# Optimization experiments

Measured on AMD Instinct MI355X. Metric: run time of the kernel, lower is better.

## Reference

```python
import jax, jax.numpy as jnp
import numpy as np

# ---- static problem configuration (mirrors Barrier_Net param) ----
B, NN, NO, SD = 100000, 16, 8, 4        # agents, neighbors, obstacles, state dim
H, PHI_OUT, ADIM = 64, 16, 2            # MLP hidden, deepset latent, action dim
DS, B_GAMMA, B_EXPH = 0.2, 0.01, 1.0    # r_safe, barrier gain, barrier exponent
PHI_MIN, PHI_MAX = -1.0, 1.0            # empty-action range
A_MIN, A_MAX = -2.0, 2.0                # final action range
D_OBS = 1 + (NN + 1) * SD + 2 * NO      # 85


def mlp2(x, w1, b1, w2, b2):
    return jax.nn.relu(x @ w1 + b1) @ w2 + b2


def setup_inputs() -> dict:
    key = jax.random.key(0)
    ks = jax.random.split(key, 10)
    x = jax.random.normal(ks[0], (B, D_OBS), jnp.float32)
    x = x.at[:, 0].set(float(NN))  # first entry encodes the neighbor count

    def w(k, shape):
        return jax.random.normal(k, shape, jnp.float32) * 0.1

    return {
        "x": x,
        "phi_w1": w(ks[1], (SD, H)), "phi_b1": jnp.zeros((H,), jnp.float32),
        "phi_w2": w(ks[2], (H, PHI_OUT)), "phi_b2": jnp.zeros((PHI_OUT,), jnp.float32),
        "obs_w1": w(ks[3], (2, H)), "obs_b1": jnp.zeros((H,), jnp.float32),
        "obs_w2": w(ks[4], (H, PHI_OUT)), "obs_b2": jnp.zeros((PHI_OUT,), jnp.float32),
        "rho_w1": w(ks[5], (PHI_OUT, H)), "rho_b1": jnp.zeros((H,), jnp.float32),
        "rho_w2": w(ks[6], (H, ADIM)), "rho_b2": jnp.zeros((ADIM,), jnp.float32),
        "psi_w1": w(ks[7], (ADIM + 2, H)), "psi_b1": jnp.zeros((H,), jnp.float32),
        "psi_w2": w(ks[8], (H, ADIM)), "psi_b2": jnp.zeros((ADIM,), jnp.float32),
    }


def reference(x, phi_w1, phi_b1, phi_w2, phi_b2, obs_w1, obs_b1, obs_w2, obs_b2,
              rho_w1, rho_b1, rho_w2, rho_b2, psi_w1, psi_b1, psi_w2, psi_b2):
    # observation layout: [nn, self(SD), nn relative neighbor states(SD each), no obstacles(2 each)]
    nb = x[:, 1 + SD:1 + SD + NN * SD].reshape(B, NN, SD)   # relative neighbor states
    ob = x[:, 1 + (NN + 1) * SD:].reshape(B, NO, 2)          # relative obstacle positions

    # --- DeepSet: permutation-invariant sum of phi over elements, then rho ---
    phi_sum = mlp2(nb, phi_w1, phi_b1, phi_w2, phi_b2).sum(axis=1)   # [B, PHI_OUT]
    obs_sum = mlp2(ob, obs_w1, obs_b1, obs_w2, obs_b2).sum(axis=1)   # [B, PHI_OUT]
    rho = mlp2(phi_sum + obs_sum, rho_w1, rho_b1, rho_w2, rho_b2)    # [B, ADIM]

    # --- empty(): psi head on cat(rho, g) with tanh range squash to [phi_min, phi_max] ---
    g = x[:, 0:2]
    e = mlp2(jnp.concatenate([rho, g], axis=1), psi_w1, psi_b1, psi_w2, psi_b2)
    empty = (jnp.tanh(e) + 1.0) * 0.5 * (PHI_MAX - PHI_MIN) + PHI_MIN

    # --- barrier: gather neighbor rel-positions, scalar potential, scatter-add per agent ---
    p_ij = -nb[..., 0:2]                                    # [B, NN, 2], p^i - p^j
    h_ij = jnp.linalg.norm(p_ij, axis=-1) - DS              # [B, NN]
    barrier = jnp.sum((B_GAMMA / h_ij ** B_EXPH)[..., None] * p_ij, axis=1)  # [B, 2]

    action = jnp.tanh(empty + barrier)
    return (action + 1.0) * 0.5 * (A_MAX - A_MIN) + A_MIN
```

## Files before the change

kernel.cpp:

```cpp
#include <hip/hip_runtime.h>

#define BATCH 100000

typedef float v2 __attribute__((ext_vector_type(2)));

__device__ __forceinline__ v2 fma2(v2 a, v2 b, v2 c) { return __builtin_elementwise_fma(a, b, c); }
__device__ __forceinline__ v2 relu2(v2 a) { v2 z = {0.f, 0.f}; return __builtin_elementwise_max(a, z); }
__device__ __forceinline__ v2 splat(float a) { v2 r = {a, a}; return r; }
__device__ __forceinline__ v2 ldv2(const float* p) { return *(const v2*)p; }

__global__ __launch_bounds__(256, 4) void barrier_net(
    const float* __restrict__ x,
    const float* __restrict__ phi_w1, const float* __restrict__ phi_b1,
    const float* __restrict__ phi_w2, const float* __restrict__ phi_b2,
    const float* __restrict__ obs_w1, const float* __restrict__ obs_b1,
    const float* __restrict__ obs_w2, const float* __restrict__ obs_b2,
    const float* __restrict__ rho_w1, const float* __restrict__ rho_b1,
    const float* __restrict__ rho_w2, const float* __restrict__ rho_b2,
    const float* __restrict__ psi_w1, const float* __restrict__ psi_b1,
    const float* __restrict__ psi_w2, const float* __restrict__ psi_b2,
    float2* __restrict__ out)
{
    __shared__ float accL[2][2][32][16];
    __shared__ float rrL[2][2][32][2];
    __shared__ float eeL[2][2][32][2];

    const int lane = threadIdx.x & 63;
    const int wave = threadIdx.x >> 6;
    const int pair = wave >> 1;
    const int h    = wave & 1;
    const int kk   = lane >> 1;
    const int t    = lane & 1;
    int s = blockIdx.x * 64 + pair * 32 + kk;
    const bool valid = (s < BATCH);
    if (!valid) s = BATCH - 1;
    const float* xr = x + (size_t)s * 85;

    const int HB = __builtin_amdgcn_readfirstlane(h) * 32;
    const float* pw1 = phi_w1 + HB;
    const float* pb1 = phi_b1 + HB;
    const float* pw2 = phi_w2 + (size_t)HB * 16;
    const float* qw1 = obs_w1 + HB;
    const float* qb1 = obs_b1 + HB;
    const float* qw2 = obs_w2 + (size_t)HB * 16;
    const float* rw1 = rho_w1 + HB;
    const float* rb1 = rho_b1 + HB;
    const float* rw2 = rho_w2 + (size_t)HB * 2;
    const float* sw1 = psi_w1 + HB;
    const float* sb1 = psi_b1 + HB;
    const float* sw2 = psi_w2 + (size_t)HB * 2;

    float nb[8][4];
    const int nbase = 5 + 32 * t;
#pragma unroll
    for (int n = 0; n < 8; ++n)
#pragma unroll
        for (int k = 0; k < 4; ++k)
            nb[n][k] = xr[nbase + 4 * n + k];

    float bar0 = 0.f, bar1 = 0.f;
    if (h == 0) {
#pragma unroll
        for (int n = 0; n < 8; ++n) {
            float p0 = -nb[n][0], p1 = -nb[n][1];
            float r  = __builtin_amdgcn_sqrtf(fmaf(p0, p0, p1 * p1));
            float sc = 0.01f * __builtin_amdgcn_rcpf(r - 0.2f);
            bar0 = fmaf(sc, p0, bar0);
            bar1 = fmaf(sc, p1, bar1);
        }
        bar0 += __shfl_xor(bar0, 1);
        bar1 += __shfl_xor(bar1, 1);
    }

    v2 acc[8];
#pragma unroll
    for (int p = 0; p < 8; ++p)
        acc[p] = fma2(splat(4.f), ldv2(phi_b2 + 2 * p),
                 fma2(splat(2.f), ldv2(obs_b2 + 2 * p), splat(0.f)));

#pragma unroll 2
    for (int c = 0; c < 4; ++c) {
        const int hb = 8 * c;
        v2 hsv[4] = {{0.f,0.f},{0.f,0.f},{0.f,0.f},{0.f,0.f}};
#pragma unroll
        for (int n = 0; n < 8; ++n) {
#pragma unroll
            for (int p = 0; p < 4; ++p) {
                v2 tv = fma2(splat(nb[n][0]), ldv2(pw1 + hb + 2 * p),
                        fma2(splat(nb[n][1]), ldv2(pw1 + 64 + hb + 2 * p),
                        fma2(splat(nb[n][2]), ldv2(pw1 + 128 + hb + 2 * p),
                        fma2(splat(nb[n][3]), ldv2(pw1 + 192 + hb + 2 * p),
                                              ldv2(pb1 + hb + 2 * p)))));
                hsv[p] += relu2(tv);
            }
        }
#pragma unroll
        for (int p = 0; p < 4; ++p) {
            const float* r0 = pw2 + (size_t)(hb + 2 * p) * 16;
            v2 hx = splat(hsv[p].x), hy = splat(hsv[p].y);
#pragma unroll
            for (int q = 0; q < 8; ++q)
                acc[q] = fma2(hy, ldv2(r0 + 16 + 2 * q),
                         fma2(hx, ldv2(r0 + 2 * q), acc[q]));
        }
    }

    float ob[4][2];
    const int obase = 69 + 8 * t;
#pragma unroll
    for (int o = 0; o < 4; ++o) {
        ob[o][0] = xr[obase + 2 * o];
        ob[o][1] = xr[obase + 2 * o + 1];
    }

#pragma unroll 2
    for (int c = 0; c < 4; ++c) {
        const int hb = 8 * c;
        v2 hsv[4] = {{0.f,0.f},{0.f,0.f},{0.f,0.f},{0.f,0.f}};
#pragma unroll
        for (int o = 0; o < 4; ++o) {
#pragma unroll
            for (int p = 0; p < 4; ++p) {
                v2 tv = fma2(splat(ob[o][0]), ldv2(qw1 + hb + 2 * p),
                        fma2(splat(ob[o][1]), ldv2(qw1 + 64 + hb + 2 * p),
                                              ldv2(qb1 + hb + 2 * p)));
                hsv[p] += relu2(tv);
            }
        }
#pragma unroll
        for (int p = 0; p < 4; ++p) {
            const float* r0 = qw2 + (size_t)(hb + 2 * p) * 16;
            v2 hx = splat(hsv[p].x), hy = splat(hsv[p].y);
#pragma unroll
            for (int q = 0; q < 8; ++q)
                acc[q] = fma2(hy, ldv2(r0 + 16 + 2 * q),
                         fma2(hx, ldv2(r0 + 2 * q), acc[q]));
        }
    }

#pragma unroll
    for (int p = 0; p < 8; ++p) {
        acc[p].x += __shfl_xor(acc[p].x, 1);
        acc[p].y += __shfl_xor(acc[p].y, 1);
    }

    {
        float* slot = &accL[pair][h][kk][8 * t];
#pragma unroll
        for (int p = 0; p < 4; ++p) {
            v2 lo = acc[p], hi = acc[p + 4];
            v2 sel;
            sel.x = t ? hi.x : lo.x;
            sel.y = t ? hi.y : lo.y;
            *(v2*)(slot + 2 * p) = sel;
        }
    }
    __syncthreads();
    {
        const float* oslot = &accL[pair][h ^ 1][kk][0];
#pragma unroll
        for (int p = 0; p < 8; ++p)
            acc[p] += ldv2(oslot + 2 * p);
    }

    const float g0 = xr[0], g1 = xr[1];

    v2 rr = (h == 0) ? ldv2(rho_b2) : splat(0.f);
#pragma unroll 2
    for (int c = 0; c < 4; ++c) {
        const int hb = 8 * c;
        v2 tt[4];
#pragma unroll
        for (int p = 0; p < 4; ++p)
            tt[p] = ldv2(rb1 + hb + 2 * p);
#pragma unroll
        for (int j = 0; j < 8; ++j) {
            v2 ax = splat(acc[j].x), ay = splat(acc[j].y);
            const float* rj0 = rw1 + (size_t)(2 * j) * 64 + hb;
            const float* rj1 = rw1 + (size_t)(2 * j + 1) * 64 + hb;
#pragma unroll
            for (int p = 0; p < 4; ++p)
                tt[p] = fma2(ay, ldv2(rj1 + 2 * p),
                        fma2(ax, ldv2(rj0 + 2 * p), tt[p]));
        }
#pragma unroll
        for (int p = 0; p < 4; ++p) {
            v2 u = relu2(tt[p]);
            rr = fma2(splat(u.x), ldv2(rw2 + 2 * (hb + 2 * p)), rr);
            rr = fma2(splat(u.y), ldv2(rw2 + 2 * (hb + 2 * p) + 2), rr);
        }
    }
    rrL[pair][h][kk][t] = t ? rr.y : rr.x;
    __syncthreads();
    {
        v2 rro = ldv2(&rrL[pair][h ^ 1][kk][0]);
        rr += rro;
    }

    v2 ee = (h == 0) ? ldv2(psi_b2) : splat(0.f);
#pragma unroll 2
    for (int c = 0; c < 4; ++c) {
        const int hb = 8 * c;
#pragma unroll
        for (int p = 0; p < 4; ++p) {
            v2 tv = fma2(splat(rr.x), ldv2(sw1 + hb + 2 * p),
                    fma2(splat(rr.y), ldv2(sw1 + 64 + hb + 2 * p),
                    fma2(splat(g0),   ldv2(sw1 + 128 + hb + 2 * p),
                    fma2(splat(g1),   ldv2(sw1 + 192 + hb + 2 * p),
                                      ldv2(sb1 + hb + 2 * p)))));
            v2 u = relu2(tv);
            ee = fma2(splat(u.x), ldv2(sw2 + 2 * (hb + 2 * p)), ee);
            ee = fma2(splat(u.y), ldv2(sw2 + 2 * (hb + 2 * p) + 2), ee);
        }
    }
    eeL[pair][h][kk][t] = t ? ee.y : ee.x;
    __syncthreads();

    if (h == 0 && t == 0 && valid) {
        v2 eeo = ldv2(&eeL[pair][1][kk][0]);
        float a0 = tanhf(tanhf(ee.x + eeo.x) + bar0);
        float a1 = tanhf(tanhf(ee.y + eeo.y) + bar1);
        out[s] = make_float2(2.f * a0, 2.f * a1);
    }
}

extern "C" void kernel_launch(void* const* d_in, const int* in_sizes, int n_in,
                              void* d_out, int out_size, void* d_ws, size_t ws_size,
                              hipStream_t stream) {
    dim3 grid((BATCH + 63) / 64), block(256);
    barrier_net<<<grid, block, 0, stream>>>(
        (const float*)d_in[0],
        (const float*)d_in[1],  (const float*)d_in[2],  (const float*)d_in[3],  (const float*)d_in[4],
        (const float*)d_in[5],  (const float*)d_in[6],  (const float*)d_in[7],  (const float*)d_in[8],
        (const float*)d_in[9],  (const float*)d_in[10], (const float*)d_in[11], (const float*)d_in[12],
        (const float*)d_in[13], (const float*)d_in[14], (const float*)d_in[15], (const float*)d_in[16],
        (float2*)d_out);
}
```

Baseline: 139.8 us.

## Stage input rows in LDS and give each lane a whole agent

The block shrinks to two waves that split the hidden dimension. Each lane now handles all 16 neighbors and 8 obstacles of one agent, instead of a lane pair splitting the elements. The block's 64 input rows are staged into padded shared memory with coalesced loads and then read back as float4 vectors, which removes the strided per-lane global loads and the shuffle reductions. In exchange each thread does twice the per-agent work and holds more registers, so latency hiding depends on the new occupancy hint.

```diff
diff --git a/kernel.cpp b/kernel.cpp
--- a/kernel.cpp
+++ b/kernel.cpp
@@ -9,7 +9,7 @@
 __device__ __forceinline__ v2 splat(float a) { v2 r = {a, a}; return r; }
 __device__ __forceinline__ v2 ldv2(const float* p) { return *(const v2*)p; }
 
-__global__ __launch_bounds__(256, 4) void barrier_net(
+__global__ __launch_bounds__(128, 3) void barrier_net(
     const float* __restrict__ x,
     const float* __restrict__ phi_w1, const float* __restrict__ phi_b1,
     const float* __restrict__ phi_w2, const float* __restrict__ phi_b2,
@@ -21,22 +21,28 @@
     const float* __restrict__ psi_w2, const float* __restrict__ psi_b2,
     float2* __restrict__ out)
 {
-    __shared__ float accL[2][2][32][16];
-    __shared__ float rrL[2][2][32][2];
-    __shared__ float eeL[2][2][32][2];
+    __shared__ float L[64 * 88];
 
     const int lane = threadIdx.x & 63;
-    const int wave = threadIdx.x >> 6;
-    const int pair = wave >> 1;
-    const int h    = wave & 1;
-    const int kk   = lane >> 1;
-    const int t    = lane & 1;
-    int s = blockIdx.x * 64 + pair * 32 + kk;
+    const int h    = threadIdx.x >> 6;
+    const int hu   = __builtin_amdgcn_readfirstlane(h);
+    const int base = blockIdx.x * 64;
+
+    for (int d = threadIdx.x; d < 64 * 85; d += 128) {
+        unsigned r = (unsigned)d / 85u;
+        int e  = d - (int)r * 85;
+        int rg = base + (int)r;
+        if (rg > BATCH - 1) rg = BATCH - 1;
+        L[(int)r * 88 + 3 + e] = x[(size_t)rg * 85 + e];
+    }
+    __syncthreads();
+
+    int s = base + lane;
     const bool valid = (s < BATCH);
     if (!valid) s = BATCH - 1;
-    const float* xr = x + (size_t)s * 85;
-
-    const int HB = __builtin_amdgcn_readfirstlane(h) * 32;
+    const float* xr = L + lane * 88 + 3;
+
+    const int HB = hu * 32;
     const float* pw1 = phi_w1 + HB;
     const float* pb1 = phi_b1 + HB;
     const float* pw2 = phi_w2 + (size_t)HB * 16;
@@ -50,40 +56,43 @@
     const float* sb1 = psi_b1 + HB;
     const float* sw2 = psi_w2 + (size_t)HB * 2;
 
-    float nb[8][4];
-    const int nbase = 5 + 32 * t;
-#pragma unroll
-    for (int n = 0; n < 8; ++n)
-#pragma unroll
-        for (int k = 0; k < 4; ++k)
-            nb[n][k] = xr[nbase + 4 * n + k];
+    const float g0 = xr[0], g1 = xr[1];
+
+    float nb[16][4];
+#pragma unroll
+    for (int n = 0; n < 16; ++n) {
+        float4 q = *(const float4*)(xr + 5 + 4 * n);
+        nb[n][0] = q.x; nb[n][1] = q.y; nb[n][2] = q.z; nb[n][3] = q.w;
+    }
 
     float bar0 = 0.f, bar1 = 0.f;
-    if (h == 0) {
-#pragma unroll
-        for (int n = 0; n < 8; ++n) {
+    if (hu == 0) {
+#pragma unroll
+        for (int n = 0; n < 16; ++n) {
             float p0 = -nb[n][0], p1 = -nb[n][1];
             float r  = __builtin_amdgcn_sqrtf(fmaf(p0, p0, p1 * p1));
             float sc = 0.01f * __builtin_amdgcn_rcpf(r - 0.2f);
             bar0 = fmaf(sc, p0, bar0);
             bar1 = fmaf(sc, p1, bar1);
         }
-        bar0 += __shfl_xor(bar0, 1);
-        bar1 += __shfl_xor(bar1, 1);
     }
 
     v2 acc[8];
 #pragma unroll
-    for (int p = 0; p < 8; ++p)
-        acc[p] = fma2(splat(4.f), ldv2(phi_b2 + 2 * p),
-                 fma2(splat(2.f), ldv2(obs_b2 + 2 * p), splat(0.f)));
+    for (int p = 0; p < 8; ++p) acc[p] = splat(0.f);
+    if (hu == 0) {
+#pragma unroll
+        for (int p = 0; p < 8; ++p)
+            acc[p] = fma2(splat(16.f), ldv2(phi_b2 + 2 * p),
+                     fma2(splat(8.f),  ldv2(obs_b2 + 2 * p), splat(0.f)));
+    }
 
 #pragma unroll 2
     for (int c = 0; c < 4; ++c) {
         const int hb = 8 * c;
         v2 hsv[4] = {{0.f,0.f},{0.f,0.f},{0.f,0.f},{0.f,0.f}};
 #pragma unroll
-        for (int n = 0; n < 8; ++n) {
+        for (int n = 0; n < 16; ++n) {
 #pragma unroll
             for (int p = 0; p < 4; ++p) {
                 v2 tv = fma2(splat(nb[n][0]), ldv2(pw1 + hb + 2 * p),
@@ -105,12 +114,12 @@
         }
     }
 
-    float ob[4][2];
-    const int obase = 69 + 8 * t;
-#pragma unroll
-    for (int o = 0; o < 4; ++o) {
-        ob[o][0] = xr[obase + 2 * o];
-        ob[o][1] = xr[obase + 2 * o + 1];
+    float ob[8][2];
+#pragma unroll
+    for (int i = 0; i < 4; ++i) {
+        float4 q = *(const float4*)(xr + 69 + 4 * i);
+        ob[2 * i][0]     = q.x; ob[2 * i][1]     = q.y;
+        ob[2 * i + 1][0] = q.z; ob[2 * i + 1][1] = q.w;
     }
 
 #pragma unroll 2
@@ -118,7 +127,7 @@
         const int hb = 8 * c;
         v2 hsv[4] = {{0.f,0.f},{0.f,0.f},{0.f,0.f},{0.f,0.f}};
 #pragma unroll
-        for (int o = 0; o < 4; ++o) {
+        for (int o = 0; o < 8; ++o) {
 #pragma unroll
             for (int p = 0; p < 4; ++p) {
                 v2 tv = fma2(splat(ob[o][0]), ldv2(qw1 + hb + 2 * p),
@@ -138,34 +147,23 @@
         }
     }
 
-#pragma unroll
-    for (int p = 0; p < 8; ++p) {
-        acc[p].x += __shfl_xor(acc[p].x, 1);
-        acc[p].y += __shfl_xor(acc[p].y, 1);
-    }
+    __syncthreads();
 
     {
-        float* slot = &accL[pair][h][kk][8 * t];
-#pragma unroll
-        for (int p = 0; p < 4; ++p) {
-            v2 lo = acc[p], hi = acc[p + 4];
-            v2 sel;
-            sel.x = t ? hi.x : lo.x;
-            sel.y = t ? hi.y : lo.y;
-            *(v2*)(slot + 2 * p) = sel;
-        }
+        float* slot = L + (h * 64 + lane) * 18;
+#pragma unroll
+        for (int p = 0; p < 8; ++p)
+            *(v2*)(slot + 2 * p) = acc[p];
     }
     __syncthreads();
     {
-        const float* oslot = &accL[pair][h ^ 1][kk][0];
+        const float* oslot = L + ((h ^ 1) * 64 + lane) * 18;
 #pragma unroll
         for (int p = 0; p < 8; ++p)
             acc[p] += ldv2(oslot + 2 * p);
     }
 
-    const float g0 = xr[0], g1 = xr[1];
-
-    v2 rr = (h == 0) ? ldv2(rho_b2) : splat(0.f);
+    v2 rr = (hu == 0) ? ldv2(rho_b2) : splat(0.f);
 #pragma unroll 2
     for (int c = 0; c < 4; ++c) {
         const int hb = 8 * c;
@@ -190,14 +188,11 @@
             rr = fma2(splat(u.y), ldv2(rw2 + 2 * (hb + 2 * p) + 2), rr);
         }
     }
-    rrL[pair][h][kk][t] = t ? rr.y : rr.x;
-    __syncthreads();
-    {
-        v2 rro = ldv2(&rrL[pair][h ^ 1][kk][0]);
-        rr += rro;
-    }
-
-    v2 ee = (h == 0) ? ldv2(psi_b2) : splat(0.f);
+    *(v2*)(L + 2304 + (h * 64 + lane) * 2) = rr;
+    __syncthreads();
+    rr += ldv2(L + 2304 + ((h ^ 1) * 64 + lane) * 2);
+
+    v2 ee = (hu == 0) ? ldv2(psi_b2) : splat(0.f);
 #pragma unroll 2
     for (int c = 0; c < 4; ++c) {
         const int hb = 8 * c;
@@ -213,13 +208,14 @@
             ee = fma2(splat(u.y), ldv2(sw2 + 2 * (hb + 2 * p) + 2), ee);
         }
     }
-    eeL[pair][h][kk][t] = t ? ee.y : ee.x;
-    __syncthreads();
-
-    if (h == 0 && t == 0 && valid) {
-        v2 eeo = ldv2(&eeL[pair][1][kk][0]);
-        float a0 = tanhf(tanhf(ee.x + eeo.x) + bar0);
-        float a1 = tanhf(tanhf(ee.y + eeo.y) + bar1);
+    if (hu == 1)
+        *(v2*)(L + 2560 + lane * 2) = ee;
+    __syncthreads();
+
+    if (hu == 0 && valid) {
+        v2 eo = ldv2(L + 2560 + lane * 2);
+        float a0 = tanhf(tanhf(ee.x + eo.x) + bar0);
+        float a1 = tanhf(tanhf(ee.y + eo.y) + bar1);
         out[s] = make_float2(2.f * a0, 2.f * a1);
     }
 }
@@ -227,7 +223,7 @@
 extern "C" void kernel_launch(void* const* d_in, const int* in_sizes, int n_in,
                               void* d_out, int out_size, void* d_ws, size_t ws_size,
                               hipStream_t stream) {
-    dim3 grid((BATCH + 63) / 64), block(256);
+    dim3 grid((BATCH + 63) / 64), block(128);
     barrier_net<<<grid, block, 0, stream>>>(
         (const float*)d_in[0],
         (const float*)d_in[1],  (const float*)d_in[2],  (const float*)d_in[3],  (const float*)d_in[4],
```

After: 143.6 us. 2.7% more time.
